# Optimization experiments

Hardware: AMD Instinct MI355X
Metric: run time of the kernel (lower is better)

## Reference

```python
import jax, jax.numpy as jnp
import numpy as np

H, W, K = 256, 256, 512
Z_THRESHOLD = 3.0
EPS = 1e-8


def setup_inputs() -> dict:
    key = jax.random.key(0)
    k1, k2, k3, k4 = jax.random.split(key, 4)
    # positions uniform in [0,H] x [0,W] x [0,64]
    positions = jax.random.uniform(k1, (K, 3)) * jnp.array([H, W, 64.0], jnp.float32)
    # scales: sigma_x, sigma_y in [1,5]; sigma_z in [0.5,2]
    s_xy = 1.0 + 4.0 * jax.random.uniform(k2, (K, 2))
    s_z = 0.5 + 1.5 * jax.random.uniform(k2, (K, 1))
    scales = jnp.concatenate([s_xy, s_z], axis=-1)
    opacity = jax.random.uniform(k3, (K,))
    intensity = jax.random.uniform(k4, (K,))
    z_target = jnp.array([32.0], jnp.float32)
    return {"positions": positions, "scales": scales, "opacity": opacity,
            "intensity": intensity, "z_target": z_target}


def reference(positions, scales, opacity, intensity, z_target):
    # z culling: instead of boolean gather (data-dependent shape), zero out
    # effective weights of culled Gaussians -> identical math (alpha=0 terms
    # contribute nothing and leave transmittance unchanged).
    z_dist = (z_target - positions[:, 2]) / (scales[:, 2] + EPS)          # (K,)
    z_mask = jnp.abs(z_dist) < Z_THRESHOLD
    z_weight = jnp.exp(-0.5 * z_dist ** 2)
    eff_w = jnp.where(z_mask, opacity * z_weight, 0.0)                    # (K,)

    grid_y = jnp.arange(H, dtype=positions.dtype)[:, None, None]         # (H,1,1)
    grid_x = jnp.arange(W, dtype=positions.dtype)[None, :, None]         # (1,W,1)
    # matches torch: dx pairs row-coord with mu_x, dy pairs col-coord with mu_y
    dxn = (grid_y - positions[:, 0]) / (scales[:, 0] + EPS)               # (H,W,K)
    dyn = (grid_x - positions[:, 1]) / (scales[:, 1] + EPS)               # (H,W,K)
    gauss = jnp.exp(-0.5 * (dxn ** 2 + dyn ** 2))                         # (H,W,K)

    # alpha compositing, sorted by weight descending
    alpha = jnp.clip(gauss * eff_w, 0.0, 0.99)
    order = jnp.argsort(-eff_w)
    alpha = alpha[:, :, order]
    s_int = intensity[order]
    trans = jnp.cumprod(1.0 - alpha, axis=-1)
    trans = jnp.concatenate([jnp.ones_like(trans[:, :, :1]), trans[:, :, :-1]], axis=-1)
    rendered = jnp.sum(trans * alpha * s_int, axis=-1)                    # (H,W)
    return rendered[None]                                                 # (1,H,W)
```

## Files before the change

### kernel.cpp

```cpp
#include <hip/hip_runtime.h>

#define IH 256
#define IW 256
#define NK 512
#define ZTH 3.0f
#define EPSV 1e-8f

__launch_bounds__(256, 4)
__global__ void slice_render_fused(const float* __restrict__ positions,
                                   const float* __restrict__ scales,
                                   const float* __restrict__ opacity,
                                   const float* __restrict__ intensity,
                                   const float* __restrict__ z_target,
                                   float* __restrict__ out) {
    __shared__ float  s_w[NK];
    __shared__ int    s_idx[NK];
    __shared__ float4 s_srt[NK + 8];
    __shared__ int    s_cnt;

    const int tid = threadIdx.x;
    const float zt = z_target[0];

    if (tid == 0) s_cnt = 0;
    __syncthreads();

    for (int k = tid; k < NK; k += 256) {
        float zd = (zt - positions[3 * k + 2]) / (scales[3 * k + 2] + EPSV);
        float w = 0.0f;
        if (fabsf(zd) < ZTH) w = opacity[k] * __expf(-0.5f * zd * zd);
        if (w > 0.0f) {
            int p = atomicAdd(&s_cnt, 1);
            s_w[p] = w;
            s_idx[p] = k;
        }
    }
    __syncthreads();

    const int m  = s_cnt;
    const int mp = (m + 7) & ~7;
    const float y = (float)blockIdx.x;

    for (int i = tid; i < mp; i += 256) {
        if (i < m) {
            float wi = s_w[i];
            int   ji = s_idx[i];
            int rank = 0;
            for (int j = 0; j < m; ++j) {
                float wj = s_w[j];
                int   jj = s_idx[j];
                rank += (wj > wi || (wj == wi && jj < ji)) ? 1 : 0;
            }
            float px  = positions[3 * ji + 0];
            float py  = positions[3 * ji + 1];
            float isx = 1.0f / (scales[3 * ji + 0] + EPSV);
            float isy = 1.0f / (scales[3 * ji + 1] + EPSV);
            float dx  = (y - px) * isx;
            float rowfac = __expf(-0.5f * dx * dx) * wi;
            s_srt[rank] = make_float4(py, isy, rowfac, intensity[ji]);
        } else {
            s_srt[i] = make_float4(0.0f, 1.0f, 0.0f, 0.0f);
        }
    }
    __syncthreads();

    const float x = (float)tid;
    float T = 1.0f, acc = 0.0f;
    for (int k0 = 0; k0 < mp; k0 += 8) {
#pragma unroll
        for (int u = 0; u < 8; ++u) {
            float4 g = s_srt[k0 + u];
            float dy = (x - g.x) * g.y;
            float a  = fminf(__expf(-0.5f * dy * dy) * g.z, 0.99f);
            acc += T * a * g.w;
            T   *= 1.0f - a;
        }
        if (__all(T < 1e-6f)) break;
    }
    out[blockIdx.x * IW + tid] = acc;
}

extern "C" void kernel_launch(void* const* d_in, const int* in_sizes, int n_in,
                              void* d_out, int out_size, void* d_ws, size_t ws_size,
                              hipStream_t stream) {
    (void)in_sizes; (void)n_in; (void)out_size; (void)d_ws; (void)ws_size;
    const float* positions = (const float*)d_in[0];
    const float* scales    = (const float*)d_in[1];
    const float* opacity   = (const float*)d_in[2];
    const float* intensity = (const float*)d_in[3];
    const float* z_target  = (const float*)d_in[4];
    float* out = (float*)d_out;
    hipLaunchKernelGGL(slice_render_fused, dim3(IH), dim3(256), 0, stream,
                       positions, scales, opacity, intensity, z_target, out);
}
```

Measured before the change: 69.69 us.

## Cull row-negligible Gaussians per row, sort by packed 64-bit keys via ballot compaction

Each block now computes each Gaussian's row factor before sorting and drops those whose row contribution is below 1e-10. Survivors are compacted with wave ballots into per-wave segments, replacing the shared atomic counter. The rank sort compares single packed 64-bit (weight, index) keys instead of a float plus a tie-break index. The composite loop unroll shrinks from 8 to 4 and the early-exit transmittance check is removed. Culling shrinks both the O(m^2) rank sort and the compositing loop, at the cost of a small approximation error. Removing the early exit may cost time when transmittance saturates.

```diff
diff --git a/kernel.cpp b/kernel.cpp
--- a/kernel.cpp
+++ b/kernel.cpp
@@ -5,6 +5,7 @@
 #define NK 512
 #define ZTH 3.0f
 #define EPSV 1e-8f
+#define RFCULL 1e-10f
 
 __launch_bounds__(256, 4)
 __global__ void slice_render_fused(const float* __restrict__ positions,
@@ -13,68 +14,84 @@
                                    const float* __restrict__ intensity,
                                    const float* __restrict__ z_target,
                                    float* __restrict__ out) {
-    __shared__ float  s_w[NK];
-    __shared__ int    s_idx[NK];
-    __shared__ float4 s_srt[NK + 8];
-    __shared__ int    s_cnt;
+    __shared__ unsigned long long s_key[NK];
+    __shared__ float4 s_g[NK];
+    __shared__ float4 s_srt[NK + 4];
+    __shared__ int    s_scnt[4];
 
-    const int tid = threadIdx.x;
+    const int tid  = threadIdx.x;
+    const int lane = tid & 63;
+    const int wid  = tid >> 6;
     const float zt = z_target[0];
+    const float y  = (float)blockIdx.x;
+    const unsigned long long ltmask = (1ull << lane) - 1ull;
 
-    if (tid == 0) s_cnt = 0;
+    int base = 0;
+    for (int r = 0; r < 2; ++r) {
+        const int k = tid + 256 * r;
+        float w = 0.0f, rowfac = 0.0f, py = 0.0f, isy = 1.0f, inten = 0.0f;
+        bool keep = false;
+        {
+            float zd = (zt - positions[3 * k + 2]) / (scales[3 * k + 2] + EPSV);
+            if (fabsf(zd) < ZTH) {
+                w = opacity[k] * __expf(-0.5f * zd * zd);
+                if (w > 0.0f) {
+                    float isx = 1.0f / (scales[3 * k + 0] + EPSV);
+                    float dx  = (y - positions[3 * k + 0]) * isx;
+                    rowfac = w * __expf(-0.5f * dx * dx);
+                    if (rowfac >= RFCULL) {
+                        keep  = true;
+                        py    = positions[3 * k + 1];
+                        isy   = 1.0f / (scales[3 * k + 1] + EPSV);
+                        inten = intensity[k];
+                    }
+                }
+            }
+        }
+        unsigned long long mask = __ballot(keep);
+        if (keep) {
+            int slot = wid * 128 + base + (int)__popcll(mask & ltmask);
+            s_key[slot] = ((unsigned long long)__float_as_uint(w) << 32)
+                          | (unsigned int)(NK - 1 - k);
+            s_g[slot] = make_float4(py, isy, rowfac, inten);
+        }
+        base += (int)__popcll(mask);
+    }
+    if (lane == 0) s_scnt[wid] = base;
     __syncthreads();
 
-    for (int k = tid; k < NK; k += 256) {
-        float zd = (zt - positions[3 * k + 2]) / (scales[3 * k + 2] + EPSV);
-        float w = 0.0f;
-        if (fabsf(zd) < ZTH) w = opacity[k] * __expf(-0.5f * zd * zd);
-        if (w > 0.0f) {
-            int p = atomicAdd(&s_cnt, 1);
-            s_w[p] = w;
-            s_idx[p] = k;
+    const int c0 = s_scnt[0], c1 = s_scnt[1], c2 = s_scnt[2], c3 = s_scnt[3];
+    const int m  = c0 + c1 + c2 + c3;
+    const int mp = (m + 3) & ~3;
+
+    for (int t = tid; t < NK; t += 256) {
+        const int seg = t >> 7, i = t & 127;
+        const int cseg = (seg == 0) ? c0 : (seg == 1) ? c1 : (seg == 2) ? c2 : c3;
+        if (i < cseg) {
+            const unsigned long long ki = s_key[t];
+            int rank = 0;
+            for (int j = 0; j < c0; ++j) rank += (s_key[      j] > ki) ? 1 : 0;
+            for (int j = 0; j < c1; ++j) rank += (s_key[128 + j] > ki) ? 1 : 0;
+            for (int j = 0; j < c2; ++j) rank += (s_key[256 + j] > ki) ? 1 : 0;
+            for (int j = 0; j < c3; ++j) rank += (s_key[384 + j] > ki) ? 1 : 0;
+            s_srt[rank] = s_g[t];
         }
     }
-    __syncthreads();
-
-    const int m  = s_cnt;
-    const int mp = (m + 7) & ~7;
-    const float y = (float)blockIdx.x;
-
-    for (int i = tid; i < mp; i += 256) {
-        if (i < m) {
-            float wi = s_w[i];
-            int   ji = s_idx[i];
-            int rank = 0;
-            for (int j = 0; j < m; ++j) {
-                float wj = s_w[j];
-                int   jj = s_idx[j];
-                rank += (wj > wi || (wj == wi && jj < ji)) ? 1 : 0;
-            }
-            float px  = positions[3 * ji + 0];
-            float py  = positions[3 * ji + 1];
-            float isx = 1.0f / (scales[3 * ji + 0] + EPSV);
-            float isy = 1.0f / (scales[3 * ji + 1] + EPSV);
-            float dx  = (y - px) * isx;
-            float rowfac = __expf(-0.5f * dx * dx) * wi;
-            s_srt[rank] = make_float4(py, isy, rowfac, intensity[ji]);
-        } else {
-            s_srt[i] = make_float4(0.0f, 1.0f, 0.0f, 0.0f);
-        }
-    }
+    for (int i = m + tid; i < mp; i += 256)
+        s_srt[i] = make_float4(0.0f, 1.0f, 0.0f, 0.0f);
     __syncthreads();
 
     const float x = (float)tid;
     float T = 1.0f, acc = 0.0f;
-    for (int k0 = 0; k0 < mp; k0 += 8) {
+    for (int k0 = 0; k0 < mp; k0 += 4) {
 #pragma unroll
-        for (int u = 0; u < 8; ++u) {
+        for (int u = 0; u < 4; ++u) {
             float4 g = s_srt[k0 + u];
             float dy = (x - g.x) * g.y;
             float a  = fminf(__expf(-0.5f * dy * dy) * g.z, 0.99f);
             acc += T * a * g.w;
             T   *= 1.0f - a;
         }
-        if (__all(T < 1e-6f)) break;
     }
     out[blockIdx.x * IW + tid] = acc;
 }
```

Result: faster. 64.84 us (-7.0%).
